# Optimization experiments

Hardware: AMD Instinct MI355X
Metric: run time of the kernel (lower is better)

The kernel has to match this reference:

```python
import jax, jax.numpy as jnp
import numpy as np

# Module constants (from init_kwargs)
B, NIN, NOUT = 128, 1024, 1024
G_OFF, G_ON, K_V = 0.001, 0.003, 0.5


def setup_inputs() -> dict:
    key = jax.random.key(0)
    k1, k2, k3 = jax.random.split(key, 3)
    stdv = 1.0 / np.sqrt(NIN)
    x = jax.random.normal(k1, (B, NIN), dtype=jnp.float32)
    # NonNeg-constrained weights, RandomNormal(mean=0.5, std=1/sqrt(in))
    w_pos = jnp.abs(0.5 + stdv * jax.random.normal(k2, (NIN, NOUT), dtype=jnp.float32))
    w_neg = jnp.abs(0.5 + stdv * jax.random.normal(k3, (NIN, NOUT), dtype=jnp.float32))
    b_pos = jnp.full((NOUT,), 0.5, dtype=jnp.float32)
    b_neg = jnp.full((NOUT,), 0.5, dtype=jnp.float32)
    return {"x": x, "w_pos": w_pos, "w_neg": w_neg, "b_pos": b_pos, "b_neg": b_neg}


def reference(x, w_pos, w_neg, b_pos, b_neg):
    # combine_weights(): append bias row, interleave pos/neg columns -> [in+1, 2*out]
    comb_pos = jnp.concatenate([w_pos, b_pos[None, :]], axis=0)  # [in+1, out]
    comb_neg = jnp.concatenate([w_neg, b_neg[None, :]], axis=0)  # [in+1, out]
    weights = jnp.stack([comb_pos, comb_neg], axis=-1).reshape(NIN + 1, 2 * NOUT)

    # append ones column for bias input; scale to voltages
    ones = jnp.ones((x.shape[0], 1), dtype=x.dtype)
    voltages = K_V * jnp.concatenate([x, ones], axis=1)  # [B, in+1]

    # double_weights_to_conductances: linear map of weights into [G_off, G_on]
    max_w = jnp.max(weights)
    k_cond = (G_ON - G_OFF) / max_w
    conductances = k_cond * weights + G_OFF  # [in+1, 2*out]

    # eval path: expand-multiply-reduce == matmul (same math, fused here)
    currents = voltages @ conductances  # [B, 2*out]

    # differential pair readout and rescale back to weight units
    total_currents = currents[:, 0::2] - currents[:, 1::2]  # [B, out]
    y_disturbed = total_currents / (K_V * k_cond)
    return y_disturbed
```

## Files before the change

kernel.cpp:

```cpp
#include <hip/hip_runtime.h>


#define NB   128
#define NIN  1024
#define NOUT 1024

#define OT   32
#define KC   64
#define NKS  (NIN / KC)
#define XP   65

__global__ __launch_bounds__(128) void memr_partial(
    const float* __restrict__ x,  const float* __restrict__ wp,
    const float* __restrict__ wn, float* __restrict__ ws)
{
    __shared__ float xs[NB * XP];
    __shared__ float wd[KC * OT];

    const int t  = threadIdx.x;
    const int o0 = blockIdx.x * OT;
    const int ks = blockIdx.y;
    const int k0 = ks * KC;

    #pragma unroll
    for (int r = 0; r < 16; ++r) {
        const int f4 = r * 128 + t;
        const int b  = f4 >> 4;
        const int q  = f4 & 15;
        const float4 v = *(const float4*)&x[(size_t)b * NIN + k0 + q * 4];
        float* d = &xs[b * XP + q * 4];
        d[0] = v.x; d[1] = v.y; d[2] = v.z; d[3] = v.w;
    }
    #pragma unroll
    for (int r = 0; r < 4; ++r) {
        const int f4 = r * 128 + t;
        const int k  = f4 >> 3;
        const int q  = f4 & 7;
        const size_t g = (size_t)(k0 + k) * NOUT + o0 + q * 4;
        const float4 p = *(const float4*)&wp[g];
        const float4 n = *(const float4*)&wn[g];
        float4 d4;
        d4.x = p.x - n.x; d4.y = p.y - n.y; d4.z = p.z - n.z; d4.w = p.w - n.w;
        *(float4*)&wd[k * OT + q * 4] = d4;
    }
    __syncthreads();

    const int tx = t & 7;
    const int ty = t >> 3;

    float acc[8][4];
    #pragma unroll
    for (int i = 0; i < 8; ++i)
        #pragma unroll
        for (int j = 0; j < 4; ++j) acc[i][j] = 0.f;

    const float* xr = &xs[ty * 8 * XP];
    const float* wr = &wd[tx * 4];

    #pragma unroll 4
    for (int k = 0; k < KC; ++k) {
        const float4 w4 = *(const float4*)&wr[k * OT];
        float xv[8];
        #pragma unroll
        for (int i = 0; i < 8; ++i) xv[i] = xr[i * XP + k];
        #pragma unroll
        for (int i = 0; i < 8; ++i) {
            acc[i][0] += xv[i] * w4.x;
            acc[i][1] += xv[i] * w4.y;
            acc[i][2] += xv[i] * w4.z;
            acc[i][3] += xv[i] * w4.w;
        }
    }

    float* wsb = ws + (size_t)ks * NB * NOUT;
    #pragma unroll
    for (int i = 0; i < 8; ++i) {
        const int b = ty * 8 + i;
        float4 v;
        v.x = acc[i][0]; v.y = acc[i][1]; v.z = acc[i][2]; v.w = acc[i][3];
        *(float4*)&wsb[(size_t)b * NOUT + o0 + tx * 4] = v;
    }
}

__global__ __launch_bounds__(256) void memr_reduce(
    const float* __restrict__ ws, const float* __restrict__ bp,
    const float* __restrict__ bn, float* __restrict__ out)
{
    const int g = blockIdx.x * 256 + threadIdx.x;
    const int o = g & (NOUT - 1);
    float s = bp[o] - bn[o];
    #pragma unroll
    for (int ks = 0; ks < NKS; ++ks)
        s += ws[(size_t)ks * NB * NOUT + g];
    out[g] = s;
}

extern "C" void kernel_launch(void* const* d_in, const int* in_sizes, int n_in,
                              void* d_out, int out_size, void* d_ws, size_t ws_size,
                              hipStream_t stream)
{
    const float* x  = (const float*)d_in[0];
    const float* wp = (const float*)d_in[1];
    const float* wn = (const float*)d_in[2];
    const float* bp = (const float*)d_in[3];
    const float* bn = (const float*)d_in[4];
    float* out = (float*)d_out;
    float* ws  = (float*)d_ws;

    dim3 g1(NOUT / OT, NKS);
    memr_partial<<<g1, 128, 0, stream>>>(x, wp, wn, ws);
    memr_reduce<<<NB * NOUT / 256, 256, 0, stream>>>(ws, bp, bn, out);
}
```

Baseline: 78.01 us.

## Transpose x tile in LDS, halve K chunk, and vectorize split-K reduction

Stores the x tile in shared memory transposed (k-major, padded to 132 floats), so each thread reads its 8 batch values with two float4 LDS loads instead of eight strided scalar loads. The K chunk is halved, which doubles the number of split-K blocks for more parallelism but also doubles the partial-sum workspace that must be written and read. The reduce kernel now processes four outputs per thread using float4 loads and stores. The trade-off is more global workspace traffic and possible bank conflicts on the transposed stores, in exchange for cheaper inner-loop LDS access and higher occupancy.

```diff
diff --git a/kernel.cpp b/kernel.cpp
--- a/kernel.cpp
+++ b/kernel.cpp
@@ -6,15 +6,15 @@
 #define NOUT 1024
 
 #define OT   32
-#define KC   64
+#define KC   32
 #define NKS  (NIN / KC)
-#define XP   65
+#define BPAD 132
 
 __global__ __launch_bounds__(128) void memr_partial(
     const float* __restrict__ x,  const float* __restrict__ wp,
     const float* __restrict__ wn, float* __restrict__ ws)
 {
-    __shared__ float xs[NB * XP];
+    __shared__ float xsT[KC * BPAD];
     __shared__ float wd[KC * OT];
 
     const int t  = threadIdx.x;
@@ -23,16 +23,18 @@
     const int k0 = ks * KC;
 
     #pragma unroll
-    for (int r = 0; r < 16; ++r) {
+    for (int r = 0; r < 8; ++r) {
         const int f4 = r * 128 + t;
-        const int b  = f4 >> 4;
-        const int q  = f4 & 15;
+        const int b  = f4 >> 3;
+        const int q  = f4 & 7;
         const float4 v = *(const float4*)&x[(size_t)b * NIN + k0 + q * 4];
-        float* d = &xs[b * XP + q * 4];
-        d[0] = v.x; d[1] = v.y; d[2] = v.z; d[3] = v.w;
+        xsT[(q * 4 + 0) * BPAD + b] = v.x;
+        xsT[(q * 4 + 1) * BPAD + b] = v.y;
+        xsT[(q * 4 + 2) * BPAD + b] = v.z;
+        xsT[(q * 4 + 3) * BPAD + b] = v.w;
     }
     #pragma unroll
-    for (int r = 0; r < 4; ++r) {
+    for (int r = 0; r < 2; ++r) {
         const int f4 = r * 128 + t;
         const int k  = f4 >> 3;
         const int q  = f4 & 7;
@@ -54,15 +56,15 @@
         #pragma unroll
         for (int j = 0; j < 4; ++j) acc[i][j] = 0.f;
 
-    const float* xr = &xs[ty * 8 * XP];
+    const float* xr = &xsT[ty * 8];
     const float* wr = &wd[tx * 4];
 
-    #pragma unroll 4
+    #pragma unroll 8
     for (int k = 0; k < KC; ++k) {
+        const float4 xa = *(const float4*)&xr[k * BPAD];
+        const float4 xb = *(const float4*)&xr[k * BPAD + 4];
         const float4 w4 = *(const float4*)&wr[k * OT];
-        float xv[8];
-        #pragma unroll
-        for (int i = 0; i < 8; ++i) xv[i] = xr[i * XP + k];
+        const float xv[8] = {xa.x, xa.y, xa.z, xa.w, xb.x, xb.y, xb.z, xb.w};
         #pragma unroll
         for (int i = 0; i < 8; ++i) {
             acc[i][0] += xv[i] * w4.x;
@@ -86,13 +88,19 @@
     const float* __restrict__ ws, const float* __restrict__ bp,
     const float* __restrict__ bn, float* __restrict__ out)
 {
-    const int g = blockIdx.x * 256 + threadIdx.x;
-    const int o = g & (NOUT - 1);
-    float s = bp[o] - bn[o];
+    const int g  = blockIdx.x * 256 + threadIdx.x;
+    const int i4 = g * 4;
+    const int o4 = i4 & (NOUT - 1);
+    const float4 p4 = *(const float4*)&bp[o4];
+    const float4 n4 = *(const float4*)&bn[o4];
+    float4 s;
+    s.x = p4.x - n4.x; s.y = p4.y - n4.y; s.z = p4.z - n4.z; s.w = p4.w - n4.w;
     #pragma unroll
-    for (int ks = 0; ks < NKS; ++ks)
-        s += ws[(size_t)ks * NB * NOUT + g];
-    out[g] = s;
+    for (int ks = 0; ks < NKS; ++ks) {
+        const float4 v = *(const float4*)&ws[(size_t)ks * NB * NOUT + i4];
+        s.x += v.x; s.y += v.y; s.z += v.z; s.w += v.w;
+    }
+    *(float4*)&out[i4] = s;
 }
 
 extern "C" void kernel_launch(void* const* d_in, const int* in_sizes, int n_in,
@@ -109,5 +117,5 @@
 
     dim3 g1(NOUT / OT, NKS);
     memr_partial<<<g1, 128, 0, stream>>>(x, wp, wn, ws);
-    memr_reduce<<<NB * NOUT / 256, 256, 0, stream>>>(ws, bp, bn, out);
+    memr_reduce<<<NB * NOUT / 4 / 256, 256, 0, stream>>>(ws, bp, bn, out);
 }
```

Measured after the change: 80.96 us. 1.04x slower.
